# Optimization experiments

Hardware: AMD Instinct MI355X
Metric: run time of the kernel (lower is better)

## Reference

```python
import jax, jax.numpy as jnp
import numpy as np

B, S, E, H = 4, 2048, 1024, 128  # batch, seq_len, n_embeddings, head_size


def setup_inputs() -> dict:
    key = jax.random.key(0)
    kx, kq, kk, kv = jax.random.split(key, 4)
    x = jax.random.normal(kx, (B, S, E), dtype=jnp.float32)
    # nn.Linear(E, H, bias=False) weights, stored transposed so proj = x @ W
    Wq = jax.random.normal(kq, (E, H), dtype=jnp.float32) * 0.02
    Wk = jax.random.normal(kk, (E, H), dtype=jnp.float32) * 0.02
    Wv = jax.random.normal(kv, (E, H), dtype=jnp.float32) * 0.02
    return {"x": x, "Wq": Wq, "Wk": Wk, "Wv": Wv}


def reference(x, Wq, Wk, Wv):
    # Single causal self-attention head (dropout = identity, eval mode).
    q = jnp.einsum("bse,eh->bsh", x, Wq)  # [B,S,H]
    k = jnp.einsum("bse,eh->bsh", x, Wk)
    v = jnp.einsum("bse,eh->bsh", x, Wv)
    scale = 1.0 / jnp.sqrt(jnp.asarray(H, dtype=x.dtype))
    scores = jnp.einsum("bqh,bkh->bqk", q, k) * scale  # [B,S,S]
    causal = jnp.tril(jnp.ones((S, S), dtype=bool))
    scores = jnp.where(causal, scores, jnp.asarray(-jnp.inf, dtype=scores.dtype))
    weights = jax.nn.softmax(scores, axis=-1)
    out = jnp.einsum("bqk,bkh->bqh", weights, v)  # [B,S,H]
    return out
```

## Files before the change

### kernel.cpp

```cpp
#include <hip/hip_runtime.h>
#include <math.h>

#define BB 4
#define SS 2048
#define EE 1024
#define HH 128
#define PLANE (BB * SS * HH)
#define BPLANE (SS * HH)
#define AUNITS 272

typedef __bf16 bf16x8 __attribute__((ext_vector_type(8)));
typedef __bf16 bf16x4 __attribute__((ext_vector_type(4)));
typedef float f32x4 __attribute__((ext_vector_type(4)));

#define QSCALE (0.08838834764831845f * 1.4426950408889634f)

__global__ __launch_bounds__(256) void prep_w(
    const float* __restrict__ Wq, const float* __restrict__ Wk,
    const float* __restrict__ Wv, __bf16* __restrict__ WT) {
  __shared__ float LT[32 * 33];
  const int p = blockIdx.x >> 7;
  const int r = blockIdx.x & 127;
  const int kb = (r >> 2) * 32, nb = (r & 3) * 32;
  const float* __restrict__ W = (p == 0) ? Wq : (p == 1) ? Wk : Wv;
  const int t = threadIdx.x;
  const int kr = t >> 3, nc4 = (t & 7) * 4;
  const float4 v = *(const float4*)&W[(size_t)(kb + kr) * HH + nb + nc4];
  LT[(nc4 + 0) * 33 + kr] = v.x;
  LT[(nc4 + 1) * 33 + kr] = v.y;
  LT[(nc4 + 2) * 33 + kr] = v.z;
  LT[(nc4 + 3) * 33 + kr] = v.w;
  __syncthreads();
  const int n = t >> 3, kc = (t & 7) * 4;
  bf16x4 o;
#pragma unroll
  for (int i = 0; i < 4; ++i) o[i] = (__bf16)LT[n * 33 + kc + i];
  *(bf16x4*)&WT[(size_t)p * (HH * EE) + (size_t)(nb + n) * EE + kb + kc] = o;
}

__global__ __launch_bounds__(256, 4) void qkv_proj(
    const float* __restrict__ x, const __bf16* __restrict__ WT,
    __bf16* __restrict__ qkv) {
  __shared__ __align__(16) __bf16 xs[32 * 72];
  __shared__ __align__(16) __bf16 wsd[128 * 72];

  const int t = threadIdx.x, w = t >> 6, lane = t & 63;
  const int quad = lane >> 4, l16 = lane & 15;
  const int mb = blockIdx.x * 32;
  const int proj = blockIdx.y;
  const __bf16* __restrict__ WTp = WT + (size_t)proj * (HH * EE);

  const int xrow0 = t >> 4, xkc0 = (t & 15) * 4;
  const int wn0 = t >> 3, wkc0 = (t & 7) * 8;

  f32x4 acc[2][2];
#pragma unroll
  for (int i = 0; i < 2; ++i)
#pragma unroll
    for (int j = 0; j < 2; ++j) acc[i][j] = (f32x4){0.f, 0.f, 0.f, 0.f};

  float4 xr[2];
  bf16x8 wr[4];
#pragma unroll
  for (int i = 0; i < 2; ++i)
    xr[i] = *(const float4*)&x[(size_t)(mb + xrow0 + i * 16) * EE + xkc0];
#pragma unroll
  for (int i = 0; i < 4; ++i)
    wr[i] = *(const bf16x8*)&WTp[(size_t)(wn0 + i * 32) * EE + wkc0];

  for (int kt = 0; kt < 16; ++kt) {
    __syncthreads();
#pragma unroll
    for (int i = 0; i < 2; ++i) {
      bf16x4 bv;
      bv[0] = (__bf16)xr[i].x; bv[1] = (__bf16)xr[i].y;
      bv[2] = (__bf16)xr[i].z; bv[3] = (__bf16)xr[i].w;
      *(bf16x4*)&xs[(xrow0 + i * 16) * 72 + xkc0] = bv;
    }
#pragma unroll
    for (int i = 0; i < 4; ++i)
      *(bf16x8*)&wsd[(wn0 + i * 32) * 72 + wkc0] = wr[i];
    __syncthreads();

    if (kt < 15) {
      const int kb = (kt + 1) * 64;
#pragma unroll
      for (int i = 0; i < 2; ++i)
        xr[i] = *(const float4*)&x[(size_t)(mb + xrow0 + i * 16) * EE + kb + xkc0];
#pragma unroll
      for (int i = 0; i < 4; ++i)
        wr[i] = *(const bf16x8*)&WTp[(size_t)(wn0 + i * 32) * EE + kb + wkc0];
    }

    bf16x8 af[2][2], bfr[2][2];
#pragma unroll
    for (int mi = 0; mi < 2; ++mi)
#pragma unroll
      for (int kc = 0; kc < 2; ++kc)
        af[mi][kc] = *(const bf16x8*)&xs[(mi * 16 + l16) * 72 + kc * 32 + quad * 8];
#pragma unroll
    for (int ni = 0; ni < 2; ++ni)
#pragma unroll
      for (int kc = 0; kc < 2; ++kc)
        bfr[ni][kc] =
            *(const bf16x8*)&wsd[(w * 32 + ni * 16 + l16) * 72 + kc * 32 + quad * 8];
#pragma unroll
    for (int kc = 0; kc < 2; ++kc)
#pragma unroll
      for (int mi = 0; mi < 2; ++mi)
#pragma unroll
        for (int ni = 0; ni < 2; ++ni)
          acc[mi][ni] = __builtin_amdgcn_mfma_f32_16x16x32_bf16(
              af[mi][kc], bfr[ni][kc], acc[mi][ni], 0, 0, 0);
  }

  if (proj < 2) {
    const float scale = (proj == 0) ? QSCALE : 1.0f;
    __bf16* outp = qkv + (size_t)proj * PLANE;
#pragma unroll
    for (int mi = 0; mi < 2; ++mi) {
      const int srow = mb + mi * 16 + quad * 4;
#pragma unroll
      for (int ni = 0; ni < 2; ++ni) {
        const int col = w * 32 + ni * 16 + l16;
#pragma unroll
        for (int rr = 0; rr < 4; ++rr)
          outp[(size_t)(srow + rr) * HH + col] = (__bf16)(acc[mi][ni][rr] * scale);
      }
    }
  } else {
    __bf16* vtp = qkv + 2 * (size_t)PLANE;
#pragma unroll
    for (int mi = 0; mi < 2; ++mi) {
      const int srow = mb + mi * 16 + quad * 4;
      const int bb = srow >> 11, sl = srow & 2047;
#pragma unroll
      for (int ni = 0; ni < 2; ++ni) {
        const int d = w * 32 + ni * 16 + l16;
        bf16x4 vv;
#pragma unroll
        for (int rr = 0; rr < 4; ++rr) vv[rr] = (__bf16)acc[mi][ni][rr];
        *(bf16x4*)&vtp[(size_t)bb * BPLANE + (size_t)d * SS + sl] = vv;
      }
    }
  }
}

__global__ __launch_bounds__(256, 3) void flash_attn_mfma(
    const __bf16* __restrict__ qkv, float* __restrict__ out,
    __bf16* __restrict__ Opart, float* __restrict__ lpart) {
  __shared__ __align__(16) __bf16 K_s[64 * 136];
  __shared__ __align__(16) __bf16 VT_s[128 * 72];

  const int t = threadIdx.x, w = t >> 6, lane = t & 63;
  const int quad = lane >> 4, l16 = lane & 15;
  const int b = blockIdx.x & 3;
  const int r = (AUNITS - 1) - (blockIdx.x >> 2);
  int tt = 0;
  while ((((tt + 2) * (tt + 2)) >> 2) <= r) ++tt;
  const int c = r - (((tt + 1) * (tt + 1)) >> 2);
  const int qrb = tt * 64;
  const int k0 = c * 128;
  const int kend = min(k0 + 128, qrb + 64);
  const int ntiles = (kend - k0) >> 6;
  const int qsb = qrb + w * 16;

  const size_t bq = (size_t)b * BPLANE;
  const __bf16* __restrict__ qp = qkv + bq;
  const __bf16* __restrict__ kp = qkv + PLANE + bq;
  const __bf16* __restrict__ vt = qkv + 2 * (size_t)PLANE + bq;

  bf16x8 qf[4];
#pragma unroll
  for (int cc = 0; cc < 4; ++cc)
    qf[cc] = *(const bf16x8*)&qp[(size_t)(qsb + l16) * HH + cc * 32 + quad * 8];

  f32x4 of[8];
#pragma unroll
  for (int f = 0; f < 8; ++f) of[f] = (f32x4){0.f, 0.f, 0.f, 0.f};
  float lp = 0.f;

  const int krow = t >> 2, kdc = (t & 3) * 8;
  bf16x8 krg[4], vrg[4];
#pragma unroll
  for (int i = 0; i < 4; ++i) {
    const int idx = t + i * 256;
    const int row = idx >> 4, dc = (idx & 15) * 8;
    krg[i] = *(const bf16x8*)&kp[(size_t)(k0 + row) * HH + dc];
  }
#pragma unroll
  for (int i = 0; i < 4; ++i) {
    const int idx = t + i * 256;
    const int d = idx >> 3, kc = (idx & 7) * 8;
    vrg[i] = *(const bf16x8*)&vt[(size_t)d * SS + k0 + kc];
  }

  for (int jt = 0; jt < ntiles; ++jt) {
    __syncthreads();
#pragma unroll
    for (int i = 0; i < 4; ++i) {
      const int idx = t + i * 256;
      const int row = idx >> 4, dc = (idx & 15) * 8;
      const int lam = (row & 32) + ((row & 4) ? 16 : 0) +
                      (((row & 31) >> 3) << 2) + (row & 3);
      *(bf16x8*)&K_s[lam * 136 + dc] = krg[i];
    }
#pragma unroll
    for (int i = 0; i < 4; ++i) {
      const int idx = t + i * 256;
      const int d = idx >> 3, kc = (idx & 7) * 8;
      *(bf16x8*)&VT_s[d * 72 + kc] = vrg[i];
    }
    __syncthreads();

    if (jt + 1 < ntiles) {
      const int kb2 = k0 + (jt + 1) * 64;
#pragma unroll
      for (int i = 0; i < 4; ++i) {
        const int idx = t + i * 256;
        const int row = idx >> 4, dc = (idx & 15) * 8;
        krg[i] = *(const bf16x8*)&kp[(size_t)(kb2 + row) * HH + dc];
      }
#pragma unroll
      for (int i = 0; i < 4; ++i) {
        const int idx = t + i * 256;
        const int d = idx >> 3, kc = (idx & 7) * 8;
        vrg[i] = *(const bf16x8*)&vt[(size_t)d * SS + kb2 + kc];
      }
    }

#pragma unroll
    for (int s32 = 0; s32 < 2; ++s32) {
      const int kabs = k0 + jt * 64 + s32 * 32;
      if (kabs <= qsb + 15) {
        bf16x8 ku[4], kv[4];
#pragma unroll
        for (int cc = 0; cc < 4; ++cc) {
          ku[cc] = *(const bf16x8*)&K_s[(s32 * 32 + l16) * 136 + cc * 32 + quad * 8];
          kv[cc] = *(const bf16x8*)&K_s[(s32 * 32 + 16 + l16) * 136 + cc * 32 + quad * 8];
        }
        f32x4 su = (f32x4){0.f, 0.f, 0.f, 0.f};
        f32x4 sv = (f32x4){0.f, 0.f, 0.f, 0.f};
#pragma unroll
        for (int cc = 0; cc < 4; ++cc) {
          su = __builtin_amdgcn_mfma_f32_16x16x32_bf16(ku[cc], qf[cc], su, 0, 0, 0);
          sv = __builtin_amdgcn_mfma_f32_16x16x32_bf16(kv[cc], qf[cc], sv, 0, 0, 0);
        }
        const int qg = qsb + l16;
        bf16x8 pa;
#pragma unroll
        for (int rr = 0; rr < 4; ++rr) {
          const int kU = kabs + quad * 8 + rr;
          const float eU = (kU <= qg) ? exp2f(su[rr]) : 0.f;
          const float eV = (kU + 4 <= qg) ? exp2f(sv[rr]) : 0.f;
          pa[rr] = (__bf16)eU;
          pa[4 + rr] = (__bf16)eV;
          lp += eU + eV;
        }
#pragma unroll
        for (int f = 0; f < 8; ++f) {
          const bf16x8 vb =
              *(const bf16x8*)&VT_s[(f * 16 + l16) * 72 + s32 * 32 + quad * 8];
          of[f] = __builtin_amdgcn_mfma_f32_16x16x32_bf16(pa, vb, of[f], 0, 0, 0);
        }
      }
    }
  }

  lp += __shfl_xor(lp, 16);
  lp += __shfl_xor(lp, 32);

  if (tt < 2) {
#pragma unroll
    for (int rr = 0; rr < 4; ++rr) {
      const float lrow = __shfl(lp, quad * 4 + rr);
      const float inv = 1.0f / lrow;
#pragma unroll
      for (int f = 0; f < 8; ++f)
        out[bq + (size_t)(qsb + quad * 4 + rr) * HH + f * 16 + l16] =
            of[f][rr] * inv;
    }
  } else {
    const int u = b * AUNITS + r;
    __bf16* op = Opart + (size_t)u * 8192;
#pragma unroll
    for (int f = 0; f < 8; ++f)
#pragma unroll
      for (int rr = 0; rr < 4; ++rr)
        op[(w * 16 + quad * 4 + rr) * 128 + f * 16 + l16] = (__bf16)of[f][rr];
    if (quad == 0) lpart[u * 64 + w * 16 + l16] = lp;
  }
}

__global__ __launch_bounds__(256) void attn_merge(
    const __bf16* __restrict__ Opart, const float* __restrict__ lpart,
    float* __restrict__ out) {
  const int b = blockIdx.x / 30;
  const int tile = 2 + (blockIdx.x % 30);
  const int nc = (tile + 2) >> 1;
  const int u0 = b * AUNITS + (((tile + 1) * (tile + 1)) >> 2);
  const int t = threadIdx.x;
#pragma unroll
  for (int i = 0; i < 4; ++i) {
    const int idx = t + i * 256;
    const int e0 = idx * 8;
    const int row = idx >> 4;
    float acc[8] = {0.f, 0.f, 0.f, 0.f, 0.f, 0.f, 0.f, 0.f};
    float lsum = 0.f;
    for (int cc = 0; cc < nc; ++cc) {
      const bf16x8 pv = *(const bf16x8*)&Opart[(size_t)(u0 + cc) * 8192 + e0];
#pragma unroll
      for (int k = 0; k < 8; ++k) acc[k] += (float)pv[k];
      lsum += lpart[(u0 + cc) * 64 + row];
    }
    const float inv = 1.0f / lsum;
    float4 r0, r1;
    r0.x = acc[0] * inv; r0.y = acc[1] * inv; r0.z = acc[2] * inv; r0.w = acc[3] * inv;
    r1.x = acc[4] * inv; r1.y = acc[5] * inv; r1.z = acc[6] * inv; r1.w = acc[7] * inv;
    float* op = out + (size_t)b * BPLANE + (size_t)tile * 8192 + e0;
    ((float4*)op)[0] = r0;
    ((float4*)op)[1] = r1;
  }
}

extern "C" void kernel_launch(void* const* d_in, const int* in_sizes, int n_in,
                              void* d_out, int out_size, void* d_ws, size_t ws_size,
                              hipStream_t stream) {
  const float* x  = (const float*)d_in[0];
  const float* Wq = (const float*)d_in[1];
  const float* Wk = (const float*)d_in[2];
  const float* Wv = (const float*)d_in[3];
  float* out = (float*)d_out;

  char* wsb = (char*)d_ws;
  __bf16* qkv = (__bf16*)wsb;
  __bf16* WT = (__bf16*)(wsb + (size_t)3 * PLANE * 2);
  __bf16* Opart = (__bf16*)(wsb + (size_t)3 * PLANE * 2 + (size_t)3 * HH * EE * 2);
  float* lpart = (float*)(wsb + (size_t)3 * PLANE * 2 + (size_t)3 * HH * EE * 2 +
                          (size_t)BB * AUNITS * 8192 * 2);

  prep_w<<<384, 256, 0, stream>>>(Wq, Wk, Wv, WT);
  qkv_proj<<<dim3(BB * SS / 32, 3), 256, 0, stream>>>(x, WT, qkv);
  flash_attn_mfma<<<BB * AUNITS, 256, 0, stream>>>(qkv, out, Opart, lpart);
  attn_merge<<<BB * 30, 256, 0, stream>>>(Opart, lpart, out);
}
```

Before: 129.0 us.

## Fuse weight prep, QKV projection, attention and merge into one cooperative kernel

Replaces the four separate launches with a single persistent cooperative kernel of 512 blocks that runs weight transpose, QKV projection, split-K flash attention and partial merge as phases separated by grid syncs. It also changes the attention work split to 192-key chunks (187 units per batch), with a matching merge, and gives the fallback merge four times more blocks. The aim is to remove launch gaps and tail effects between kernels, at the cost of grid-wide barriers, a fixed block count of two blocks per CU, and the risk of load imbalance within phases.

```diff
diff --git a/kernel.cpp b/kernel.cpp
--- a/kernel.cpp
+++ b/kernel.cpp
@@ -1,5 +1,8 @@
 #include <hip/hip_runtime.h>
+#include <hip/hip_cooperative_groups.h>
 #include <math.h>
+
+namespace cg = cooperative_groups;
 
 #define BB 4
 #define SS 2048
@@ -7,6 +10,9 @@
 #define HH 128
 #define PLANE (BB * SS * HH)
 #define BPLANE (SS * HH)
+#define UPB_C 187
+#define NU_C (UPB_C * 4)
+#define NBLK_C 512
 #define AUNITS 272
 
 typedef __bf16 bf16x8 __attribute__((ext_vector_type(8)));
@@ -14,6 +20,326 @@
 typedef float f32x4 __attribute__((ext_vector_type(4)));
 
 #define QSCALE (0.08838834764831845f * 1.4426950408889634f)
+
+__global__ __launch_bounds__(256, 2) void fused_head(
+    const float* __restrict__ x, const float* __restrict__ Wq,
+    const float* __restrict__ Wk, const float* __restrict__ Wv,
+    __bf16* __restrict__ qkv, __bf16* __restrict__ WT,
+    __bf16* __restrict__ Opart, float* __restrict__ lpart,
+    float* __restrict__ out) {
+  cg::grid_group grid = cg::this_grid();
+  __shared__ __align__(16) char smem[35840];
+
+  const int t = threadIdx.x, w = t >> 6, lane = t & 63;
+  const int quad = lane >> 4, l16 = lane & 15;
+  const int u = blockIdx.x;
+
+  if (u < 384) {
+    float* LT = (float*)smem;
+    const int p = u >> 7;
+    const int r0 = u & 127;
+    const int kb = (r0 >> 2) * 32, nb = (r0 & 3) * 32;
+    const float* __restrict__ W = (p == 0) ? Wq : (p == 1) ? Wk : Wv;
+    const int kr = t >> 3, nc4 = (t & 7) * 4;
+    const float4 v = *(const float4*)&W[(size_t)(kb + kr) * HH + nb + nc4];
+    LT[(nc4 + 0) * 33 + kr] = v.x;
+    LT[(nc4 + 1) * 33 + kr] = v.y;
+    LT[(nc4 + 2) * 33 + kr] = v.z;
+    LT[(nc4 + 3) * 33 + kr] = v.w;
+    __syncthreads();
+    const int n = t >> 3, kc = (t & 7) * 4;
+    bf16x4 o;
+#pragma unroll
+    for (int i = 0; i < 4; ++i) o[i] = (__bf16)LT[n * 33 + kc + i];
+    *(bf16x4*)&WT[(size_t)p * (HH * EE) + (size_t)(nb + n) * EE + kb + kc] = o;
+  }
+  __threadfence();
+  grid.sync();
+
+  for (int uu = u; uu < 768; uu += NBLK_C) {
+    __bf16* xs = (__bf16*)smem;
+    __bf16* wsd = (__bf16*)(smem + 4608);
+    const int mb = (uu & 255) * 32;
+    const int proj = uu >> 8;
+    const __bf16* __restrict__ WTp = WT + (size_t)proj * (HH * EE);
+
+    const int xrow0 = t >> 4, xkc0 = (t & 15) * 4;
+    const int wn0 = t >> 3, wkc0 = (t & 7) * 8;
+
+    f32x4 acc[2][2];
+#pragma unroll
+    for (int i = 0; i < 2; ++i)
+#pragma unroll
+      for (int j = 0; j < 2; ++j) acc[i][j] = (f32x4){0.f, 0.f, 0.f, 0.f};
+
+    float4 xr[2];
+    bf16x8 wr[4];
+#pragma unroll
+    for (int i = 0; i < 2; ++i)
+      xr[i] = *(const float4*)&x[(size_t)(mb + xrow0 + i * 16) * EE + xkc0];
+#pragma unroll
+    for (int i = 0; i < 4; ++i)
+      wr[i] = *(const bf16x8*)&WTp[(size_t)(wn0 + i * 32) * EE + wkc0];
+
+    for (int kt = 0; kt < 16; ++kt) {
+      __syncthreads();
+#pragma unroll
+      for (int i = 0; i < 2; ++i) {
+        bf16x4 bv;
+        bv[0] = (__bf16)xr[i].x; bv[1] = (__bf16)xr[i].y;
+        bv[2] = (__bf16)xr[i].z; bv[3] = (__bf16)xr[i].w;
+        *(bf16x4*)&xs[(xrow0 + i * 16) * 72 + xkc0] = bv;
+      }
+#pragma unroll
+      for (int i = 0; i < 4; ++i)
+        *(bf16x8*)&wsd[(wn0 + i * 32) * 72 + wkc0] = wr[i];
+      __syncthreads();
+
+      if (kt < 15) {
+        const int kb = (kt + 1) * 64;
+#pragma unroll
+        for (int i = 0; i < 2; ++i)
+          xr[i] = *(const float4*)&x[(size_t)(mb + xrow0 + i * 16) * EE + kb + xkc0];
+#pragma unroll
+        for (int i = 0; i < 4; ++i)
+          wr[i] = *(const bf16x8*)&WTp[(size_t)(wn0 + i * 32) * EE + kb + wkc0];
+      }
+
+      bf16x8 af[2][2], bfr[2][2];
+#pragma unroll
+      for (int mi = 0; mi < 2; ++mi)
+#pragma unroll
+        for (int kc = 0; kc < 2; ++kc)
+          af[mi][kc] = *(const bf16x8*)&xs[(mi * 16 + l16) * 72 + kc * 32 + quad * 8];
+#pragma unroll
+      for (int ni = 0; ni < 2; ++ni)
+#pragma unroll
+        for (int kc = 0; kc < 2; ++kc)
+          bfr[ni][kc] =
+              *(const bf16x8*)&wsd[(w * 32 + ni * 16 + l16) * 72 + kc * 32 + quad * 8];
+#pragma unroll
+      for (int kc = 0; kc < 2; ++kc)
+#pragma unroll
+        for (int mi = 0; mi < 2; ++mi)
+#pragma unroll
+          for (int ni = 0; ni < 2; ++ni)
+            acc[mi][ni] = __builtin_amdgcn_mfma_f32_16x16x32_bf16(
+                af[mi][kc], bfr[ni][kc], acc[mi][ni], 0, 0, 0);
+    }
+
+    if (proj < 2) {
+      const float scale = (proj == 0) ? QSCALE : 1.0f;
+      __bf16* outp = qkv + (size_t)proj * PLANE;
+#pragma unroll
+      for (int mi = 0; mi < 2; ++mi) {
+        const int srow = mb + mi * 16 + quad * 4;
+#pragma unroll
+        for (int ni = 0; ni < 2; ++ni) {
+          const int col = w * 32 + ni * 16 + l16;
+#pragma unroll
+          for (int rr = 0; rr < 4; ++rr)
+            outp[(size_t)(srow + rr) * HH + col] = (__bf16)(acc[mi][ni][rr] * scale);
+        }
+      }
+    } else {
+      __bf16* vtp = qkv + 2 * (size_t)PLANE;
+#pragma unroll
+      for (int mi = 0; mi < 2; ++mi) {
+        const int srow = mb + mi * 16 + quad * 4;
+        const int bb2 = srow >> 11, sl = srow & 2047;
+#pragma unroll
+        for (int ni = 0; ni < 2; ++ni) {
+          const int d = w * 32 + ni * 16 + l16;
+          bf16x4 vv;
+#pragma unroll
+          for (int rr = 0; rr < 4; ++rr) vv[rr] = (__bf16)acc[mi][ni][rr];
+          *(bf16x4*)&vtp[(size_t)bb2 * BPLANE + (size_t)d * SS + sl] = vv;
+        }
+      }
+    }
+    __syncthreads();
+  }
+  __threadfence();
+  grid.sync();
+
+  for (int uu = u; uu < NU_C; uu += NBLK_C) {
+    __bf16* K_s = (__bf16*)smem;
+    __bf16* VT_s = (__bf16*)(smem + 17408);
+    const int ur = (NU_C - 1) - uu;
+    const int b = ur & 3;
+    const int r = ur >> 2;
+    int tt = 0, Pp = 0;
+    for (;;) {
+      const int n = (tt + 3) / 3;
+      if (r < Pp + n) break;
+      Pp += n;
+      ++tt;
+    }
+    const int c = r - Pp;
+    const int qrb = tt * 64;
+    const int k0 = c * 192;
+    const int kend = min(k0 + 192, qrb + 64);
+    const int ntiles = (kend - k0 + 63) >> 6;
+    const int qsb = qrb + w * 16;
+
+    const size_t bq = (size_t)b * BPLANE;
+    const __bf16* __restrict__ qp = qkv + bq;
+    const __bf16* __restrict__ kp = qkv + PLANE + bq;
+    const __bf16* __restrict__ vt = qkv + 2 * (size_t)PLANE + bq;
+
+    bf16x8 qf[4];
+#pragma unroll
+    for (int cc = 0; cc < 4; ++cc)
+      qf[cc] = *(const bf16x8*)&qp[(size_t)(qsb + l16) * HH + cc * 32 + quad * 8];
+
+    f32x4 of[8];
+#pragma unroll
+    for (int f = 0; f < 8; ++f) of[f] = (f32x4){0.f, 0.f, 0.f, 0.f};
+    float lp = 0.f;
+
+    bf16x8 krg[4], vrg[4];
+#pragma unroll
+    for (int i = 0; i < 4; ++i) {
+      const int idx = t + i * 256;
+      const int row = idx >> 4, dc = (idx & 15) * 8;
+      krg[i] = *(const bf16x8*)&kp[(size_t)(k0 + row) * HH + dc];
+    }
+#pragma unroll
+    for (int i = 0; i < 4; ++i) {
+      const int idx = t + i * 256;
+      const int d = idx >> 3, kc = (idx & 7) * 8;
+      vrg[i] = *(const bf16x8*)&vt[(size_t)d * SS + k0 + kc];
+    }
+
+    for (int jt = 0; jt < ntiles; ++jt) {
+      __syncthreads();
+#pragma unroll
+      for (int i = 0; i < 4; ++i) {
+        const int idx = t + i * 256;
+        const int row = idx >> 4, dc = (idx & 15) * 8;
+        const int lam = (row & 32) + ((row & 4) ? 16 : 0) +
+                        (((row & 31) >> 3) << 2) + (row & 3);
+        *(bf16x8*)&K_s[lam * 136 + dc] = krg[i];
+      }
+#pragma unroll
+      for (int i = 0; i < 4; ++i) {
+        const int idx = t + i * 256;
+        const int d = idx >> 3, kc = (idx & 7) * 8;
+        *(bf16x8*)&VT_s[d * 72 + kc] = vrg[i];
+      }
+      __syncthreads();
+
+      if (jt + 1 < ntiles) {
+        const int kb2 = k0 + (jt + 1) * 64;
+#pragma unroll
+        for (int i = 0; i < 4; ++i) {
+          const int idx = t + i * 256;
+          const int row = idx >> 4, dc = (idx & 15) * 8;
+          krg[i] = *(const bf16x8*)&kp[(size_t)(kb2 + row) * HH + dc];
+        }
+#pragma unroll
+        for (int i = 0; i < 4; ++i) {
+          const int idx = t + i * 256;
+          const int d = idx >> 3, kc = (idx & 7) * 8;
+          vrg[i] = *(const bf16x8*)&vt[(size_t)d * SS + kb2 + kc];
+        }
+      }
+
+#pragma unroll
+      for (int s32 = 0; s32 < 2; ++s32) {
+        const int kabs = k0 + jt * 64 + s32 * 32;
+        if (kabs <= qsb + 15) {
+          bf16x8 ku[4], kv[4];
+#pragma unroll
+          for (int cc = 0; cc < 4; ++cc) {
+            ku[cc] = *(const bf16x8*)&K_s[(s32 * 32 + l16) * 136 + cc * 32 + quad * 8];
+            kv[cc] = *(const bf16x8*)&K_s[(s32 * 32 + 16 + l16) * 136 + cc * 32 + quad * 8];
+          }
+          f32x4 su = (f32x4){0.f, 0.f, 0.f, 0.f};
+          f32x4 sv = (f32x4){0.f, 0.f, 0.f, 0.f};
+#pragma unroll
+          for (int cc = 0; cc < 4; ++cc) {
+            su = __builtin_amdgcn_mfma_f32_16x16x32_bf16(ku[cc], qf[cc], su, 0, 0, 0);
+            sv = __builtin_amdgcn_mfma_f32_16x16x32_bf16(kv[cc], qf[cc], sv, 0, 0, 0);
+          }
+          const int qg = qsb + l16;
+          bf16x8 pa;
+#pragma unroll
+          for (int rr = 0; rr < 4; ++rr) {
+            const int kU = kabs + quad * 8 + rr;
+            const float eU = (kU <= qg) ? exp2f(su[rr]) : 0.f;
+            const float eV = (kU + 4 <= qg) ? exp2f(sv[rr]) : 0.f;
+            pa[rr] = (__bf16)eU;
+            pa[4 + rr] = (__bf16)eV;
+            lp += eU + eV;
+          }
+#pragma unroll
+          for (int f = 0; f < 8; ++f) {
+            const bf16x8 vb =
+                *(const bf16x8*)&VT_s[(f * 16 + l16) * 72 + s32 * 32 + quad * 8];
+            of[f] = __builtin_amdgcn_mfma_f32_16x16x32_bf16(pa, vb, of[f], 0, 0, 0);
+          }
+        }
+      }
+    }
+
+    lp += __shfl_xor(lp, 16);
+    lp += __shfl_xor(lp, 32);
+
+    if (tt < 3) {
+#pragma unroll
+      for (int rr = 0; rr < 4; ++rr) {
+        const float lrow = __shfl(lp, quad * 4 + rr);
+        const float inv = 1.0f / lrow;
+#pragma unroll
+        for (int f = 0; f < 8; ++f)
+          out[bq + (size_t)(qsb + quad * 4 + rr) * HH + f * 16 + l16] =
+              of[f][rr] * inv;
+      }
+    } else {
+      const int us = b * UPB_C + r;
+      __bf16* op = Opart + (size_t)us * 8192;
+#pragma unroll
+      for (int f = 0; f < 8; ++f)
+#pragma unroll
+        for (int rr = 0; rr < 4; ++rr)
+          op[(w * 16 + quad * 4 + rr) * 128 + f * 16 + l16] = (__bf16)of[f][rr];
+      if (quad == 0) lpart[us * 64 + w * 16 + l16] = lp;
+    }
+    __syncthreads();
+  }
+  __threadfence();
+  grid.sync();
+
+  if (u < 464) {
+    const int q4 = u & 3;
+    const int m = u >> 2;
+    const int b = m / 29;
+    const int tile = 3 + (m % 29);
+    const int nc = (tile + 3) / 3;
+    int Pp = 0;
+    for (int j = 0; j < tile; ++j) Pp += (j + 3) / 3;
+    const int u0 = b * UPB_C + Pp;
+    const int idx = q4 * 256 + t;
+    const int e0 = idx * 8;
+    const int row = idx >> 4;
+    float acc[8] = {0.f, 0.f, 0.f, 0.f, 0.f, 0.f, 0.f, 0.f};
+    float lsum = 0.f;
+    for (int cc = 0; cc < nc; ++cc) {
+      const bf16x8 pv = *(const bf16x8*)&Opart[(size_t)(u0 + cc) * 8192 + e0];
+#pragma unroll
+      for (int k = 0; k < 8; ++k) acc[k] += (float)pv[k];
+      lsum += lpart[(u0 + cc) * 64 + row];
+    }
+    const float inv = 1.0f / lsum;
+    float4 r0, r1;
+    r0.x = acc[0] * inv; r0.y = acc[1] * inv; r0.z = acc[2] * inv; r0.w = acc[3] * inv;
+    r1.x = acc[4] * inv; r1.y = acc[5] * inv; r1.z = acc[6] * inv; r1.w = acc[7] * inv;
+    float* op = out + (size_t)b * BPLANE + (size_t)tile * 8192 + e0;
+    ((float4*)op)[0] = r0;
+    ((float4*)op)[1] = r1;
+  }
+}
 
 __global__ __launch_bounds__(256) void prep_w(
     const float* __restrict__ Wq, const float* __restrict__ Wk,
@@ -133,14 +459,14 @@
 #pragma unroll
     for (int mi = 0; mi < 2; ++mi) {
       const int srow = mb + mi * 16 + quad * 4;
-      const int bb = srow >> 11, sl = srow & 2047;
+      const int bb2 = srow >> 11, sl = srow & 2047;
 #pragma unroll
       for (int ni = 0; ni < 2; ++ni) {
         const int d = w * 32 + ni * 16 + l16;
         bf16x4 vv;
 #pragma unroll
         for (int rr = 0; rr < 4; ++rr) vv[rr] = (__bf16)acc[mi][ni][rr];
-        *(bf16x4*)&vtp[(size_t)bb * BPLANE + (size_t)d * SS + sl] = vv;
+        *(bf16x4*)&vtp[(size_t)bb2 * BPLANE + (size_t)d * SS + sl] = vv;
       }
     }
   }
@@ -180,7 +506,6 @@
   for (int f = 0; f < 8; ++f) of[f] = (f32x4){0.f, 0.f, 0.f, 0.f};
   float lp = 0.f;
 
-  const int krow = t >> 2, kdc = (t & 3) * 8;
   bf16x8 krg[4], vrg[4];
 #pragma unroll
   for (int i = 0; i < 4; ++i) {
@@ -295,32 +620,30 @@
 __global__ __launch_bounds__(256) void attn_merge(
     const __bf16* __restrict__ Opart, const float* __restrict__ lpart,
     float* __restrict__ out) {
-  const int b = blockIdx.x / 30;
-  const int tile = 2 + (blockIdx.x % 30);
+  const int q4 = blockIdx.x & 3;
+  const int m = blockIdx.x >> 2;
+  const int b = m / 30;
+  const int tile = 2 + (m % 30);
   const int nc = (tile + 2) >> 1;
   const int u0 = b * AUNITS + (((tile + 1) * (tile + 1)) >> 2);
-  const int t = threadIdx.x;
-#pragma unroll
-  for (int i = 0; i < 4; ++i) {
-    const int idx = t + i * 256;
-    const int e0 = idx * 8;
-    const int row = idx >> 4;
-    float acc[8] = {0.f, 0.f, 0.f, 0.f, 0.f, 0.f, 0.f, 0.f};
-    float lsum = 0.f;
-    for (int cc = 0; cc < nc; ++cc) {
-      const bf16x8 pv = *(const bf16x8*)&Opart[(size_t)(u0 + cc) * 8192 + e0];
-#pragma unroll
-      for (int k = 0; k < 8; ++k) acc[k] += (float)pv[k];
-      lsum += lpart[(u0 + cc) * 64 + row];
-    }
-    const float inv = 1.0f / lsum;
-    float4 r0, r1;
-    r0.x = acc[0] * inv; r0.y = acc[1] * inv; r0.z = acc[2] * inv; r0.w = acc[3] * inv;
-    r1.x = acc[4] * inv; r1.y = acc[5] * inv; r1.z = acc[6] * inv; r1.w = acc[7] * inv;
-    float* op = out + (size_t)b * BPLANE + (size_t)tile * 8192 + e0;
-    ((float4*)op)[0] = r0;
-    ((float4*)op)[1] = r1;
-  }
+  const int idx = q4 * 256 + threadIdx.x;
+  const int e0 = idx * 8;
+  const int row = idx >> 4;
+  float acc[8] = {0.f, 0.f, 0.f, 0.f, 0.f, 0.f, 0.f, 0.f};
+  float lsum = 0.f;
+  for (int cc = 0; cc < nc; ++cc) {
+    const bf16x8 pv = *(const bf16x8*)&Opart[(size_t)(u0 + cc) * 8192 + e0];
+#pragma unroll
+    for (int k = 0; k < 8; ++k) acc[k] += (float)pv[k];
+    lsum += lpart[(u0 + cc) * 64 + row];
+  }
+  const float inv = 1.0f / lsum;
+  float4 r0, r1;
+  r0.x = acc[0] * inv; r0.y = acc[1] * inv; r0.z = acc[2] * inv; r0.w = acc[3] * inv;
+  r1.x = acc[4] * inv; r1.y = acc[5] * inv; r1.z = acc[6] * inv; r1.w = acc[7] * inv;
+  float* op = out + (size_t)b * BPLANE + (size_t)tile * 8192 + e0;
+  ((float4*)op)[0] = r0;
+  ((float4*)op)[1] = r1;
 }
 
 extern "C" void kernel_launch(void* const* d_in, const int* in_sizes, int n_in,
@@ -339,8 +662,25 @@
   float* lpart = (float*)(wsb + (size_t)3 * PLANE * 2 + (size_t)3 * HH * EE * 2 +
                           (size_t)BB * AUNITS * 8192 * 2);
 
-  prep_w<<<384, 256, 0, stream>>>(Wq, Wk, Wv, WT);
-  qkv_proj<<<dim3(BB * SS / 32, 3), 256, 0, stream>>>(x, WT, qkv);
-  flash_attn_mfma<<<BB * AUNITS, 256, 0, stream>>>(qkv, out, Opart, lpart);
-  attn_merge<<<BB * 30, 256, 0, stream>>>(Opart, lpart, out);
+  int dev = 0;
+  (void)hipGetDevice(&dev);
+  int coop = 0, ncu = 0, maxb = 0;
+  (void)hipDeviceGetAttribute(&coop, hipDeviceAttributeCooperativeLaunch, dev);
+  (void)hipDeviceGetAttribute(&ncu, hipDeviceAttributeMultiprocessorCount, dev);
+  (void)hipOccupancyMaxActiveBlocksPerMultiprocessor(&maxb, (const void*)fused_head,
+                                                     256, 0);
+  const bool use_coop = (coop != 0) && ((long)maxb * ncu >= NBLK_C);
+
+  if (use_coop) {
+    void* args[] = {(void*)&x, (void*)&Wq, (void*)&Wk, (void*)&Wv,
+                    (void*)&qkv, (void*)&WT, (void*)&Opart, (void*)&lpart,
+                    (void*)&out};
+    hipLaunchCooperativeKernel((void*)fused_head, dim3(NBLK_C), dim3(256), args,
+                               0, stream);
+  } else {
+    prep_w<<<384, 256, 0, stream>>>(Wq, Wk, Wv, WT);
+    qkv_proj<<<dim3(BB * SS / 32, 3), 256, 0, stream>>>(x, WT, qkv);
+    flash_attn_mfma<<<BB * AUNITS, 256, 0, stream>>>(qkv, out, Opart, lpart);
+    attn_merge<<<BB * 30 * 4, 256, 0, stream>>>(Opart, lpart, out);
+  }
 }
```

Result: faster. 114.9 us (-11.0%).
